# Performance work log

Measured on AMD Instinct MI355X. Metric: run time of the kernel, lower is better.

The kernel has to match this reference:

```python
import jax, jax.numpy as jnp
import numpy as np

EMBED_DIM = 128
NUM_HEADS = 16
D_K = EMBED_DIM // NUM_HEADS  # must equal n_wires = 8


def setup_inputs() -> dict:
    key = jax.random.key(0)
    k1, k2 = jax.random.split(key)
    x = jax.random.normal(k1, (8, 2048, EMBED_DIM), dtype=jnp.float32)
    theta = jax.random.normal(k2, (D_K,), dtype=jnp.float32)  # trainable RX angles, one per wire
    return {"x": x, "theta": theta}


def _quantum_measure(q, theta):
    # q: [B, H, S, 8]. RX(x)RX(theta) = RX(x+theta); product state gives <Z_i> = cos(phi_i).
    # CNOT chain C(0,1)..C(6,7),C(7,0) in Heisenberg picture:
    #   <Z_0> = prod_{i=1..7} cos(phi_i);  <Z_w> = prod_{i=0..w} cos(phi_i), w>=1.
    c = jnp.cos(q + theta)                       # [B,H,S,8]
    cp = jnp.cumprod(c, axis=-1)                 # prefix products prod_{0..w}
    z0 = jnp.prod(c[..., 1:], axis=-1, keepdims=True)
    return jnp.concatenate([z0, cp[..., 1:]], axis=-1)  # [B,H,S,8]


def reference(x, theta):
    B, S, E = x.shape
    # split heads: [B,S,E] -> [B,H,S,d_k]
    q = x.reshape(B, S, NUM_HEADS, D_K).transpose(0, 2, 1, 3)
    out = _quantum_measure(q, theta)             # [B,H,S,8]
    # merge heads back: [B,S,E]
    out = out.transpose(0, 2, 1, 3).reshape(B, S, E)
    scores = jnp.einsum('bse,bte->bst', out, out) / jnp.sqrt(jnp.float32(D_K))
    attn = jax.nn.softmax(scores, axis=-1)       # dropout = identity in eval mode
    return jnp.einsum('bst,bte->bse', attn, out)
```

## Files before the change

### kernel.cpp

```cpp
#include <hip/hip_runtime.h>

#define NB 8
#define SS 2048
#define DD 128
#define SCALE 0.35355339059327373f

typedef _Float16 f16x8 __attribute__((ext_vector_type(8)));
typedef float f32x16 __attribute__((ext_vector_type(16)));
typedef unsigned short u16;
typedef u16 u16x8 __attribute__((ext_vector_type(8)));

__device__ __forceinline__ unsigned pkrtz(float a, float b) {
    unsigned w;
    asm("v_cvt_pkrtz_f16_f32 %0, %1, %2" : "=v"(w) : "v"(a), "v"(b));
    return w;
}

__device__ __forceinline__ void gload_lds16(const u16* g, u16* l) {
    __builtin_amdgcn_global_load_lds(
        (const __attribute__((address_space(1))) unsigned*)g,
        (__attribute__((address_space(3))) unsigned*)l, 16, 0, 0);
}

__global__ __launch_bounds__(512) void qmeasure_kernel(const float* __restrict__ x,
                                                       const float* __restrict__ theta,
                                                       u16* __restrict__ G1,
                                                       u16* __restrict__ G2) {
    __shared__ u16 olds[32][128];
    const int bid = blockIdx.x;
    const int b = bid & 7;
    const int t = bid >> 3;
    const int tid = threadIdx.x;
    const int s = tid >> 4;
    const int c = tid & 15;

    float th[8];
    *(float4*)th = *(const float4*)theta;
    *(float4*)(th + 4) = *(const float4*)(theta + 4);

    const float* xp = x + (((size_t)b * SS + t * 32 + s) * DD) + c * 8;
    float4 a = *(const float4*)xp;
    float4 a2 = *(const float4*)(xp + 4);
    float cc[8];
    cc[0] = __cosf(a.x + th[0]);  cc[1] = __cosf(a.y + th[1]);
    cc[2] = __cosf(a.z + th[2]);  cc[3] = __cosf(a.w + th[3]);
    cc[4] = __cosf(a2.x + th[4]); cc[5] = __cosf(a2.y + th[5]);
    cc[6] = __cosf(a2.z + th[6]); cc[7] = __cosf(a2.w + th[7]);
    float o[8];
    o[1] = cc[0] * cc[1];
    o[2] = o[1] * cc[2]; o[3] = o[2] * cc[3]; o[4] = o[3] * cc[4];
    o[5] = o[4] * cc[5]; o[6] = o[5] * cc[6]; o[7] = o[6] * cc[7];
    float z = cc[1] * cc[2]; z *= cc[3]; z *= cc[4]; z *= cc[5]; z *= cc[6]; z *= cc[7];
    o[0] = z;

    u16x8 w;
#pragma unroll
    for (int e = 0; e < 8; ++e) w[e] = __builtin_bit_cast(u16, (_Float16)o[e]);

    {
        const int chunk = t * 512 + (c >> 1) * 64 + (c & 1) * 32 + s;
        *(u16x8*)(G1 + (size_t)b * (SS * DD) + (size_t)chunk * 8) = w;
    }
    *(u16x8*)&olds[s][c * 8] = w;
    __syncthreads();
    {
        const int lo5 = tid & 31;
        const int hi = (tid >> 5) & 1;
        const int dkc = tid >> 6;
        const int dt = dkc >> 1, kc2 = dkc & 1;
        u16x8 g;
#pragma unroll
        for (int u = 0; u < 8; ++u) g[u] = olds[kc2 * 16 + hi * 8 + u][dt * 32 + lo5];
        const int chunk = t * 512 + dkc * 64 + hi * 32 + lo5;
        *(u16x8*)(G2 + (size_t)b * (SS * DD) + (size_t)chunk * 8) = g;
    }
}

__global__ __launch_bounds__(512, 2) void qattn_kernel(const u16* __restrict__ G1g,
                                                       const u16* __restrict__ G2g,
                                                       float* __restrict__ out) {
    __shared__ __align__(16) u16 sb[2][2][4][4096];

    const int tid = threadIdx.x;
    const int lane = tid & 63;
    const int wave = tid >> 6;
    const int lo5 = lane & 31;
    const int hi = lane >> 5;
    const int qw = wave & 1;
    const int kq = wave >> 1;
    const int bid = blockIdx.x;
    const int b = bid & 7;
    const int qg = bid >> 3;

    const u16* G1b = G1g + (size_t)b * (SS * DD);
    const u16* G2b = G2g + (size_t)b * (SS * DD);

    f16x8 qf[8];
    {
        const u16* qp = G1b + (size_t)(qg * 2 + qw) * 4096 + lane * 8;
#pragma unroll
        for (int kc = 0; kc < 8; ++kc) qf[kc] = *(const f16x8*)(qp + kc * 512);
    }

    f32x16 accT[4];
#pragma unroll
    for (int dt = 0; dt < 4; ++dt)
#pragma unroll
        for (int e = 0; e < 16; ++e) accT[dt][e] = 0.f;
    float m = -3.0e38f, l = 0.f;

    {
        const int t = kq * 16;
        const u16* src = (qw == 0 ? G1b : G2b) + (size_t)t * 4096 + lane * 8;
        u16* dst = &sb[0][qw][kq][0];
#pragma unroll
        for (int w = 0; w < 8; ++w) gload_lds16(src + w * 512, dst + w * 512);
    }
    __syncthreads();

    for (int it = 0; it < 16; ++it) {
        const int cur = it & 1;
        if (it < 15) {
            const int t = kq * 16 + it + 1;
            const u16* src = (qw == 0 ? G1b : G2b) + (size_t)t * 4096 + lane * 8;
            u16* dst = &sb[cur ^ 1][qw][kq][0];
#pragma unroll
            for (int w = 0; w < 8; ++w) gload_lds16(src + w * 512, dst + w * 512);
        }

        const u16* Kb = &sb[cur][0][kq][0];
        const u16* Vb = &sb[cur][1][kq][0];

        f16x8 kf[8];
#pragma unroll
        for (int kc = 0; kc < 8; ++kc) kf[kc] = *(const f16x8*)(Kb + kc * 512 + lane * 8);

        f32x16 acc;
#pragma unroll
        for (int e = 0; e < 16; ++e) acc[e] = 0.f;
#pragma unroll
        for (int kc = 0; kc < 8; ++kc)
            acc = __builtin_amdgcn_mfma_f32_32x32x16_f16(kf[kc], qf[kc], acc, 0, 0, 0);

        f16x8 vf[8];
#pragma unroll
        for (int j = 0; j < 8; ++j) vf[j] = *(const f16x8*)(Vb + j * 512 + lane * 8);

        float tmax = acc[0];
#pragma unroll
        for (int r = 1; r < 16; ++r) tmax = fmaxf(tmax, acc[r]);
        tmax *= SCALE;
        tmax = fmaxf(tmax, __shfl_xor(tmax, 32));
        if (!__all(tmax <= m + 8.f)) {
            const float mnew = fmaxf(m, tmax);
            const float corr = __expf(m - mnew);
            l *= corr;
#pragma unroll
            for (int dt = 0; dt < 4; ++dt)
#pragma unroll
                for (int e = 0; e < 16; ++e) accT[dt][e] *= corr;
            m = mnew;
        }
        float rowsum = 0.f;
#pragma unroll
        for (int r = 0; r < 16; ++r) {
            float p = __expf(acc[r] * SCALE - m);
            acc[r] = p;
            rowsum += p;
        }
        rowsum += __shfl_xor(rowsum, 32);
        l += rowsum;

        f16x8 pa[2];
#pragma unroll
        for (int kc2 = 0; kc2 < 2; ++kc2) {
            const int r0 = kc2 * 8;
            unsigned w0 = pkrtz(acc[r0 + 0], acc[r0 + 1]);
            unsigned w2 = pkrtz(acc[r0 + 4], acc[r0 + 5]);
            asm("v_permlane32_swap_b32 %0, %1" : "+v"(w0), "+v"(w2));
            unsigned w1 = pkrtz(acc[r0 + 2], acc[r0 + 3]);
            unsigned w3 = pkrtz(acc[r0 + 6], acc[r0 + 7]);
            asm("v_permlane32_swap_b32 %0, %1" : "+v"(w1), "+v"(w3));
            union { unsigned w[4]; f16x8 v; } u;
            u.w[0] = w0; u.w[1] = w1; u.w[2] = w2; u.w[3] = w3;
            pa[kc2] = u.v;
        }

#pragma unroll
        for (int dt = 0; dt < 4; ++dt) {
            f32x16 a = accT[dt];
#pragma unroll
            for (int kc2 = 0; kc2 < 2; ++kc2)
                a = __builtin_amdgcn_mfma_f32_32x32x16_f16(vf[dt * 2 + kc2], pa[kc2], a, 0, 0, 0);
            accT[dt] = a;
        }

        __syncthreads();
    }

    float* obuf = (float*)(&sb[0][0][0][0]);
    float* mlb = (float*)((unsigned char*)(&sb[0][0][0][0]) + 49152);
    float* orow = out + ((size_t)b * SS + qg * 64 + qw * 32 + lo5) * DD;
#pragma unroll
    for (int half = 0; half < 2; ++half) {
        if (kq > 0) {
            if (half == 0 && hi == 0) {
                mlb[((qw * 3 + (kq - 1)) * 2 + 0) * 32 + lo5] = m;
                mlb[((qw * 3 + (kq - 1)) * 2 + 1) * 32 + lo5] = l;
            }
#pragma unroll
            for (int dh = 0; dh < 2; ++dh)
#pragma unroll
                for (int r = 0; r < 16; ++r)
                    obuf[(((qw * 3 + (kq - 1)) * 2 + dh) * 16 + r) * 64 + lane] =
                        accT[half * 2 + dh][r];
        }
        __syncthreads();
        if (kq == 0) {
            const float mj0 = mlb[((qw * 3 + 0) * 2 + 0) * 32 + lo5];
            const float lj0 = mlb[((qw * 3 + 0) * 2 + 1) * 32 + lo5];
            const float mj1 = mlb[((qw * 3 + 1) * 2 + 0) * 32 + lo5];
            const float lj1 = mlb[((qw * 3 + 1) * 2 + 1) * 32 + lo5];
            const float mj2 = mlb[((qw * 3 + 2) * 2 + 0) * 32 + lo5];
            const float lj2 = mlb[((qw * 3 + 2) * 2 + 1) * 32 + lo5];
            const float ms = fmaxf(fmaxf(m, mj0), fmaxf(mj1, mj2));
            const float w0 = __expf(m - ms), w1 = __expf(mj0 - ms);
            const float w2 = __expf(mj1 - ms), w3 = __expf(mj2 - ms);
            const float linv = 1.f / (l * w0 + lj0 * w1 + lj1 * w2 + lj2 * w3);
#pragma unroll
            for (int dh = 0; dh < 2; ++dh) {
                const int dt = half * 2 + dh;
#pragma unroll
                for (int r = 0; r < 16; ++r) {
                    const float o = accT[dt][r] * w0 +
                                    obuf[(((qw * 3 + 0) * 2 + dh) * 16 + r) * 64 + lane] * w1 +
                                    obuf[(((qw * 3 + 1) * 2 + dh) * 16 + r) * 64 + lane] * w2 +
                                    obuf[(((qw * 3 + 2) * 2 + dh) * 16 + r) * 64 + lane] * w3;
                    const int drow = (r & 3) + 8 * (r >> 2) + 4 * hi;
                    orow[dt * 32 + drow] = o * linv;
                }
            }
        }
        __syncthreads();
    }
}

extern "C" void kernel_launch(void* const* d_in, const int* in_sizes, int n_in,
                              void* d_out, int out_size, void* d_ws, size_t ws_size,
                              hipStream_t stream) {
    const float* x = (const float*)d_in[0];
    const float* theta = (const float*)d_in[1];
    float* outp = (float*)d_out;
    u16* G1 = (u16*)d_ws;
    u16* G2 = G1 + (size_t)NB * SS * DD;

    qmeasure_kernel<<<512, 512, 0, stream>>>(x, theta, G1, G2);
    qattn_kernel<<<256, 512, 0, stream>>>(G1, G2, outp);
}
```

Before: 36.29 us.

## Replace direct global-to-LDS loads with register-staged prefetch pipeline and wave priorities

The K/V tile staging switches from global_load_lds DMA to plain global loads into registers two tiles ahead, then stores them to LDS one iteration later, with explicit barriers and waitcnt. K and V fragments are now read from LDS right next to the MFMAs that use them instead of being preloaded, and s_setprio is raised around the MFMA blocks. The max and sum reductions are restructured into trees, and qmeasure now writes G1 through padded LDS to get coalesced stores. This adds register pressure and relies on hand-placed synchronization (lgkmcnt waits only for LDS, not vmcnt) in exchange for deeper latency hiding.

```diff
diff --git a/kernel.cpp b/kernel.cpp
--- a/kernel.cpp
+++ b/kernel.cpp
@@ -16,17 +16,11 @@
     return w;
 }
 
-__device__ __forceinline__ void gload_lds16(const u16* g, u16* l) {
-    __builtin_amdgcn_global_load_lds(
-        (const __attribute__((address_space(1))) unsigned*)g,
-        (__attribute__((address_space(3))) unsigned*)l, 16, 0, 0);
-}
-
 __global__ __launch_bounds__(512) void qmeasure_kernel(const float* __restrict__ x,
                                                        const float* __restrict__ theta,
                                                        u16* __restrict__ G1,
                                                        u16* __restrict__ G2) {
-    __shared__ u16 olds[32][128];
+    __shared__ u16 olds[32][136];
     const int bid = blockIdx.x;
     const int b = bid & 7;
     const int t = bid >> 3;
@@ -56,22 +50,25 @@
     u16x8 w;
 #pragma unroll
     for (int e = 0; e < 8; ++e) w[e] = __builtin_bit_cast(u16, (_Float16)o[e]);
-
-    {
-        const int chunk = t * 512 + (c >> 1) * 64 + (c & 1) * 32 + s;
-        *(u16x8*)(G1 + (size_t)b * (SS * DD) + (size_t)chunk * 8) = w;
-    }
     *(u16x8*)&olds[s][c * 8] = w;
     __syncthreads();
+
+    {
+        const int kc = tid >> 6, hh = (tid >> 5) & 1, r = tid & 31;
+        u16x8 g;
+#pragma unroll
+        for (int u = 0; u < 8; ++u) g[u] = olds[r][kc * 16 + hh * 8 + u];
+        *(u16x8*)(G1 + (size_t)b * (SS * DD) + ((size_t)t * 512 + tid) * 8) = g;
+    }
     {
         const int lo5 = tid & 31;
-        const int hi = (tid >> 5) & 1;
+        const int hh = (tid >> 5) & 1;
         const int dkc = tid >> 6;
         const int dt = dkc >> 1, kc2 = dkc & 1;
         u16x8 g;
 #pragma unroll
-        for (int u = 0; u < 8; ++u) g[u] = olds[kc2 * 16 + hi * 8 + u][dt * 32 + lo5];
-        const int chunk = t * 512 + dkc * 64 + hi * 32 + lo5;
+        for (int u = 0; u < 8; ++u) g[u] = olds[kc2 * 16 + hh * 8 + u][dt * 32 + lo5];
+        const int chunk = t * 512 + dkc * 64 + hh * 32 + lo5;
         *(u16x8*)(G2 + (size_t)b * (SS * DD) + (size_t)chunk * 8) = g;
     }
 }
@@ -94,6 +91,7 @@
 
     const u16* G1b = G1g + (size_t)b * (SS * DD);
     const u16* G2b = G2g + (size_t)b * (SS * DD);
+    const u16* sbase = (qw ? G2b : G1b);
 
     f16x8 qf[8];
     {
@@ -109,47 +107,63 @@
         for (int e = 0; e < 16; ++e) accT[dt][e] = 0.f;
     float m = -3.0e38f, l = 0.f;
 
-    {
-        const int t = kq * 16;
-        const u16* src = (qw == 0 ? G1b : G2b) + (size_t)t * 4096 + lane * 8;
-        u16* dst = &sb[0][qw][kq][0];
-#pragma unroll
-        for (int w = 0; w < 8; ++w) gload_lds16(src + w * 512, dst + w * 512);
-    }
-    __syncthreads();
+    f16x8 sreg[8];
+    {
+        const u16* src = sbase + (size_t)(kq * 16) * 4096 + lane * 8;
+#pragma unroll
+        for (int w = 0; w < 8; ++w) sreg[w] = *(const f16x8*)(src + w * 512);
+        u16* dst = &sb[0][qw][kq][0] + lane * 8;
+#pragma unroll
+        for (int w = 0; w < 8; ++w) *(f16x8*)(dst + w * 512) = sreg[w];
+        const u16* src1 = sbase + (size_t)(kq * 16 + 1) * 4096 + lane * 8;
+#pragma unroll
+        for (int w = 0; w < 8; ++w) sreg[w] = *(const f16x8*)(src1 + w * 512);
+    }
+    asm volatile("s_waitcnt lgkmcnt(0)" ::: "memory");
+    __builtin_amdgcn_sched_barrier(0);
+    __builtin_amdgcn_s_barrier();
 
     for (int it = 0; it < 16; ++it) {
         const int cur = it & 1;
+        if (it >= 1) {
+        }
         if (it < 15) {
-            const int t = kq * 16 + it + 1;
-            const u16* src = (qw == 0 ? G1b : G2b) + (size_t)t * 4096 + lane * 8;
-            u16* dst = &sb[cur ^ 1][qw][kq][0];
-#pragma unroll
-            for (int w = 0; w < 8; ++w) gload_lds16(src + w * 512, dst + w * 512);
-        }
-
-        const u16* Kb = &sb[cur][0][kq][0];
-        const u16* Vb = &sb[cur][1][kq][0];
-
-        f16x8 kf[8];
-#pragma unroll
-        for (int kc = 0; kc < 8; ++kc) kf[kc] = *(const f16x8*)(Kb + kc * 512 + lane * 8);
+            u16* dst = &sb[cur ^ 1][qw][kq][0] + lane * 8;
+#pragma unroll
+            for (int w = 0; w < 8; ++w) *(f16x8*)(dst + w * 512) = sreg[w];
+            if (it < 14) {
+                const u16* src = sbase + (size_t)(kq * 16 + it + 2) * 4096 + lane * 8;
+#pragma unroll
+                for (int w = 0; w < 8; ++w) sreg[w] = *(const f16x8*)(src + w * 512);
+            }
+            asm volatile("s_waitcnt lgkmcnt(0)" ::: "memory");
+            __builtin_amdgcn_sched_barrier(0);
+        }
+        __builtin_amdgcn_s_barrier();
+        __builtin_amdgcn_sched_barrier(0);
+
+        const u16* Kb = &sb[cur][0][kq][0] + lane * 8;
+        const u16* Vb = &sb[cur][1][kq][0] + lane * 8;
 
         f32x16 acc;
 #pragma unroll
         for (int e = 0; e < 16; ++e) acc[e] = 0.f;
-#pragma unroll
-        for (int kc = 0; kc < 8; ++kc)
-            acc = __builtin_amdgcn_mfma_f32_32x32x16_f16(kf[kc], qf[kc], acc, 0, 0, 0);
-
-        f16x8 vf[8];
-#pragma unroll
-        for (int j = 0; j < 8; ++j) vf[j] = *(const f16x8*)(Vb + j * 512 + lane * 8);
-
-        float tmax = acc[0];
-#pragma unroll
-        for (int r = 1; r < 16; ++r) tmax = fmaxf(tmax, acc[r]);
-        tmax *= SCALE;
+        __builtin_amdgcn_s_setprio(1);
+#pragma unroll
+        for (int kc = 0; kc < 8; ++kc) {
+            f16x8 kf = *(const f16x8*)(Kb + kc * 512);
+            acc = __builtin_amdgcn_mfma_f32_32x32x16_f16(kf, qf[kc], acc, 0, 0, 0);
+        }
+        __builtin_amdgcn_s_setprio(0);
+
+        float ma = fmaxf(fmaxf(acc[0], acc[1]), acc[2]);
+        float mb = fmaxf(fmaxf(acc[8], acc[9]), acc[10]);
+        ma = fmaxf(fmaxf(ma, acc[3]), acc[4]);
+        mb = fmaxf(fmaxf(mb, acc[11]), acc[12]);
+        ma = fmaxf(fmaxf(ma, acc[5]), acc[6]);
+        mb = fmaxf(fmaxf(mb, acc[13]), acc[14]);
+        ma = fmaxf(fmaxf(ma, acc[7]), mb);
+        float tmax = fmaxf(ma, acc[15]) * SCALE;
         tmax = fmaxf(tmax, __shfl_xor(tmax, 32));
         if (!__all(tmax <= m + 8.f)) {
             const float mnew = fmaxf(m, tmax);
@@ -161,13 +175,13 @@
                 for (int e = 0; e < 16; ++e) accT[dt][e] *= corr;
             m = mnew;
         }
-        float rowsum = 0.f;
-#pragma unroll
-        for (int r = 0; r < 16; ++r) {
-            float p = __expf(acc[r] * SCALE - m);
-            acc[r] = p;
-            rowsum += p;
-        }
+#pragma unroll
+        for (int r = 0; r < 16; ++r) acc[r] = __expf(acc[r] * SCALE - m);
+        float s0 = (acc[0] + acc[1]) + (acc[2] + acc[3]);
+        float s1 = (acc[4] + acc[5]) + (acc[6] + acc[7]);
+        float s2 = (acc[8] + acc[9]) + (acc[10] + acc[11]);
+        float s3 = (acc[12] + acc[13]) + (acc[14] + acc[15]);
+        float rowsum = (s0 + s1) + (s2 + s3);
         rowsum += __shfl_xor(rowsum, 32);
         l += rowsum;
 
@@ -186,18 +200,24 @@
             pa[kc2] = u.v;
         }
 
+        __builtin_amdgcn_s_setprio(1);
 #pragma unroll
         for (int dt = 0; dt < 4; ++dt) {
             f32x16 a = accT[dt];
 #pragma unroll
-            for (int kc2 = 0; kc2 < 2; ++kc2)
-                a = __builtin_amdgcn_mfma_f32_32x32x16_f16(vf[dt * 2 + kc2], pa[kc2], a, 0, 0, 0);
+            for (int kc2 = 0; kc2 < 2; ++kc2) {
+                f16x8 vf = *(const f16x8*)(Vb + (dt * 2 + kc2) * 512);
+                a = __builtin_amdgcn_mfma_f32_32x32x16_f16(vf, pa[kc2], a, 0, 0, 0);
+            }
             accT[dt] = a;
         }
-
-        __syncthreads();
-    }
-
+        __builtin_amdgcn_s_setprio(0);
+
+        __builtin_amdgcn_sched_barrier(0);
+        __builtin_amdgcn_s_barrier();
+    }
+
+    __syncthreads();
     float* obuf = (float*)(&sb[0][0][0][0]);
     float* mlb = (float*)((unsigned char*)(&sb[0][0][0][0]) + 49152);
     float* orow = out + ((size_t)b * SS + qg * 64 + qw * 32 + lo5) * DD;
```

After: 40.16 us. 10.7% more time.
